# Kernel optimization log

Measured on AMD Instinct MI355X. Metric: run time of the kernel, lower is better.

The kernel has to match this reference:

```python
import jax, jax.numpy as jnp
import numpy as np

B, S, E, H = 4, 2048, 1024, 16
D = E // H


def setup_inputs() -> dict:
    key = jax.random.key(0)
    ks = jax.random.split(key, 8)
    inv = 1.0 / np.sqrt(E)
    return {
        "query": jax.random.normal(ks[0], (B, S, E), dtype=jnp.float32),
        "key": jax.random.normal(ks[1], (B, S, E), dtype=jnp.float32),
        "value": jax.random.normal(ks[2], (B, S, E), dtype=jnp.float32),
        "key_padding_mask": jnp.zeros((B, S), dtype=bool),
        "Wq": jax.random.uniform(ks[3], (E, E), jnp.float32, -inv, inv),
        "Wk": jax.random.uniform(ks[4], (E, E), jnp.float32, -inv, inv),
        "Wv": jax.random.uniform(ks[5], (E, E), jnp.float32, -inv, inv),
        "Wo": jax.random.uniform(ks[6], (E, E), jnp.float32, -inv, inv),
        "gamma": jnp.ones((H,), dtype=jnp.float32),
    }


def reference(query, key, value, key_padding_mask, Wq, Wk, Wv, Wo, gamma):
    b, s, e = query.shape
    h = gamma.shape[0]
    d = e // h
    # torch Linear: x @ W.T ; split into heads -> [b, h, s, d]
    q = (query @ Wq.T).reshape(b, s, h, d).swapaxes(1, 2)
    k = (key @ Wk.T).reshape(b, key.shape[1], h, d).swapaxes(1, 2)
    v = (value @ Wv.T).reshape(b, value.shape[1], h, d).swapaxes(1, 2)
    scores = jnp.einsum("bhqd,bhkd->bhqk", q, k) / jnp.sqrt(jnp.asarray(d, q.dtype))
    scores = jnp.where(key_padding_mask[:, None, None, :], -jnp.inf, scores)
    attn = jax.nn.softmax(scores, axis=-1)  # dropout p=0 in eval-equivalent reference
    out = jnp.einsum("bhqk,bhkd->bhqd", attn, v)
    out = out * gamma[None, :, None, None]  # head-scale
    out = out.swapaxes(1, 2).reshape(b, s, e)
    return out @ Wo.T
```

## Files before the change

kernel.cpp:

```cpp
#include <hip/hip_runtime.h>
#include <hip/hip_bf16.h>
#include <cstdint>

typedef __bf16 bf16;
typedef __bf16 bf16_8 __attribute__((ext_vector_type(8)));
typedef __bf16 bf16_4 __attribute__((ext_vector_type(4)));
typedef float f32_4 __attribute__((ext_vector_type(4)));
typedef short s16x4 __attribute__((ext_vector_type(4)));
typedef short s16x8 __attribute__((ext_vector_type(8)));

#define MFMA_16x16x32(a, b, c) __builtin_amdgcn_mfma_f32_16x16x32_bf16((a), (b), (c), 0, 0, 0)

__device__ __forceinline__ void gll16(const void* g, void* l) {
  __builtin_amdgcn_global_load_lds((const __attribute__((address_space(1))) void*)g,
                                   (__attribute__((address_space(3))) void*)l, 16, 0, 0);
}

__device__ __forceinline__ float exp2fast(float x) {
#if __has_builtin(__builtin_amdgcn_exp2f)
  return __builtin_amdgcn_exp2f(x);
#else
  return __exp2f(x);
#endif
}

__device__ __forceinline__ unsigned bfbits(float x) {
  bf16 b = (bf16)x;
  return (unsigned)__builtin_bit_cast(unsigned short, b);
}

__device__ __forceinline__ bf16_8 cvt8(float4 a, float4 b) {
  bf16_8 v;
  v[0] = (bf16)a.x; v[1] = (bf16)a.y; v[2] = (bf16)a.z; v[3] = (bf16)a.w;
  v[4] = (bf16)b.x; v[5] = (bf16)b.y; v[6] = (bf16)b.z; v[7] = (bf16)b.w;
  return v;
}

__global__ __launch_bounds__(256) void convert4(const float* __restrict__ w0,
                                                const float* __restrict__ w1,
                                                const float* __restrict__ w2,
                                                const float* __restrict__ w3,
                                                bf16* __restrict__ out, int per) {
  const float* srcs[4] = {w0, w1, w2, w3};
  const float* src = srcs[blockIdx.y];
  bf16* dst = out + (size_t)blockIdx.y * per;
  const float sc = (blockIdx.y == 0) ? 0.18033688f : 1.0f;
  int i = (blockIdx.x * 256 + threadIdx.x) * 4;
  float4 f = *(const float4*)(src + i);
  bf16_4 v;
  v[0] = (bf16)(f.x * sc); v[1] = (bf16)(f.y * sc);
  v[2] = (bf16)(f.z * sc); v[3] = (bf16)(f.w * sc);
  *(bf16_4*)(dst + i) = v;
}

__global__ __launch_bounds__(256) void gemm_qkv(const float* __restrict__ Aq,
                                                const float* __restrict__ Ak,
                                                const float* __restrict__ Av,
                                                const bf16* __restrict__ W,
                                                bf16* __restrict__ Qp,
                                                bf16* __restrict__ Kp,
                                                bf16* __restrict__ Vt) {
  constexpr int BM = 128, BK = 32, K = 1024, N = 1024, M_S = 2048;
  __shared__ alignas(16) bf16 As[2][BM * BK];
  __shared__ alignas(16) bf16 Bs[2][BM * BK];

  const int tid = threadIdx.x;
  const int wave = tid >> 6, lane = tid & 63;
  const int quad = lane >> 4, l15 = lane & 15;
  const int wm = (wave & 1) * 64, wn = (wave >> 1) * 64;
  const int tensor = blockIdx.y >> 3;
  const int n0 = (blockIdx.y & 7) * 128;
  const size_t m0 = (size_t)blockIdx.x * BM;

  const float* A = tensor == 0 ? Aq : (tensor == 1 ? Ak : Av);
  const bf16* Bt = W + ((size_t)tensor << 20);

  f32_4 acc[4][4] = {};

  const size_t g_laneoff = (size_t)(lane >> 2) * K + (lane & 3) * 8;
  const float* Ag = A + (m0 + wave * 32) * (size_t)K + g_laneoff;
  const bf16* Bg = Bt + ((size_t)n0 + wave * 32) * (size_t)K + g_laneoff;
  const int l_off = wave * 32 * BK + lane * 8;

  auto stageB = [&](int b, int k0) {
    gll16(Bg + k0, &Bs[b][l_off]);
    gll16(Bg + 16 * (size_t)K + k0, &Bs[b][l_off + 16 * BK]);
  };
  auto loadA = [&](int k0, float4* r) {
    r[0] = *(const float4*)(Ag + k0);
    r[1] = *(const float4*)(Ag + k0 + 4);
    r[2] = *(const float4*)(Ag + 16 * (size_t)K + k0);
    r[3] = *(const float4*)(Ag + 16 * (size_t)K + k0 + 4);
  };
  auto writeA = [&](int b, const float4* r) {
    *(bf16_8*)&As[b][l_off] = cvt8(r[0], r[1]);
    *(bf16_8*)&As[b][l_off + 16 * BK] = cvt8(r[2], r[3]);
  };

  {
    float4 a0[4];
    loadA(0, a0);
    stageB(0, 0);
    writeA(0, a0);
  }
  int buf = 0;
  for (int k0 = 0; k0 < K; k0 += BK, buf ^= 1) {
    __syncthreads();
    const bool more = k0 + BK < K;
    float4 an[4];
    if (more) {
      loadA(k0 + BK, an);
      stageB(buf ^ 1, k0 + BK);
    }

    bf16_8 af[4], bfr[4];
#pragma unroll
    for (int mt = 0; mt < 4; ++mt)
      af[mt] = *(const bf16_8*)&As[buf][(wm + mt * 16 + l15) * BK + quad * 8];
#pragma unroll
    for (int nt = 0; nt < 4; ++nt)
      bfr[nt] = *(const bf16_8*)&Bs[buf][(wn + nt * 16 + l15) * BK + quad * 8];
#pragma unroll
    for (int mt = 0; mt < 4; ++mt)
#pragma unroll
      for (int nt = 0; nt < 4; ++nt)
        acc[mt][nt] = MFMA_16x16x32(af[mt], bfr[nt], acc[mt][nt]);

    if (more) writeA(buf ^ 1, an);
  }

  if (tensor < 2) {
    bf16* C = tensor == 0 ? Qp : Kp;
#pragma unroll
    for (int mt = 0; mt < 4; ++mt)
#pragma unroll
      for (int i = 0; i < 4; ++i) {
        size_t row = m0 + wm + mt * 16 + quad * 4 + i;
        bf16* cr = C + row * N + n0 + wn + l15;
#pragma unroll
        for (int nt = 0; nt < 4; ++nt) cr[nt * 16] = (bf16)acc[mt][nt][i];
      }
  } else {
    const int bb = (int)(m0 >> 11);
    const int sbase = (int)(m0 & 2047) + wm;
#pragma unroll
    for (int mt = 0; mt < 4; ++mt)
#pragma unroll
      for (int nt = 0; nt < 4; ++nt) {
        int col = n0 + wn + nt * 16 + l15;
        bf16_4 pk;
        pk[0] = (bf16)acc[mt][nt][0]; pk[1] = (bf16)acc[mt][nt][1];
        pk[2] = (bf16)acc[mt][nt][2]; pk[3] = (bf16)acc[mt][nt][3];
        bf16* dst = Vt + ((size_t)(bb * 16 + (col >> 6)) * 64 + (col & 63)) * M_S +
                    sbase + (mt >> 1) * 32 + quad * 8 + (mt & 1) * 4;
        *(bf16_4*)dst = pk;
      }
  }
}

__global__ __launch_bounds__(256) void gemm_out(const bf16* __restrict__ A,
                                                const bf16* __restrict__ Bt,
                                                float* __restrict__ C,
                                                int M, int N, int K) {
  constexpr int BM = 128, BN = 128, BK = 32;
  __shared__ alignas(16) bf16 As[2][BM * BK];
  __shared__ alignas(16) bf16 Bs[2][BN * BK];

  const int tid = threadIdx.x;
  const int wave = tid >> 6, lane = tid & 63;
  const int quad = lane >> 4, l15 = lane & 15;
  const int wm = (wave & 1) * 64, wn = (wave >> 1) * 64;
  const size_t m0 = (size_t)blockIdx.x * BM;
  const size_t n0 = (size_t)blockIdx.y * BN;

  f32_4 acc[4][4] = {};

  const size_t g_laneoff = (size_t)(lane >> 2) * K + (lane & 3) * 8;
  const bf16* Ag = A + (m0 + wave * 32) * (size_t)K + g_laneoff;
  const bf16* Bg = Bt + (n0 + wave * 32) * (size_t)K + g_laneoff;
  const int l_off = wave * 32 * BK + lane * 8;

  auto stage = [&](int b, int k0) {
    gll16(Ag + k0, &As[b][l_off]);
    gll16(Ag + 16 * (size_t)K + k0, &As[b][l_off + 16 * BK]);
    gll16(Bg + k0, &Bs[b][l_off]);
    gll16(Bg + 16 * (size_t)K + k0, &Bs[b][l_off + 16 * BK]);
  };

  stage(0, 0);
  int buf = 0;
  for (int k0 = 0; k0 < K; k0 += BK, buf ^= 1) {
    __syncthreads();
    if (k0 + BK < K) stage(buf ^ 1, k0 + BK);

    bf16_8 af[4], bfr[4];
#pragma unroll
    for (int mt = 0; mt < 4; ++mt)
      af[mt] = *(const bf16_8*)&As[buf][(wm + mt * 16 + l15) * BK + quad * 8];
#pragma unroll
    for (int nt = 0; nt < 4; ++nt)
      bfr[nt] = *(const bf16_8*)&Bs[buf][(wn + nt * 16 + l15) * BK + quad * 8];
#pragma unroll
    for (int mt = 0; mt < 4; ++mt)
#pragma unroll
      for (int nt = 0; nt < 4; ++nt)
        acc[mt][nt] = MFMA_16x16x32(af[mt], bfr[nt], acc[mt][nt]);
  }

#pragma unroll
  for (int mt = 0; mt < 4; ++mt)
#pragma unroll
    for (int i = 0; i < 4; ++i) {
      size_t row = m0 + wm + mt * 16 + quad * 4 + i;
      float* cr = C + row * N + n0 + wn + l15;
#pragma unroll
      for (int nt = 0; nt < 4; ++nt) cr[nt * 16] = acc[mt][nt][i];
    }
}

__global__ __launch_bounds__(256, 4) void attn_fused(const bf16* __restrict__ Q,
                                                     const bf16* __restrict__ K,
                                                     const bf16* __restrict__ Vt,
                                                     const unsigned char* __restrict__ mask,
                                                     const float* __restrict__ gamma,
                                                     bf16* __restrict__ Out) {
  constexpr int S = 2048, E = 1024;
  constexpr float NEGB = -3.0e38f;
  __shared__ alignas(16) bf16 Ks[2][64 * 64];
  __shared__ alignas(16) bf16 Vs[2][64 * 64];

  const int tid = threadIdx.x;
  const int wave = tid >> 6, lane = tid & 63;
  const int quad = lane >> 4, l15 = lane & 15;

  const int bx = blockIdx.x, by = blockIdx.y;
  const int wx = (bx >> 3) | ((by & 7) << 1);
  const int bh = (bx & 7) | (by & ~7);
  const int q0 = wx * 128;
  const int b = bh >> 4, h = bh & 15;

  const unsigned char* mg = mask + (size_t)b * S;

  bool anym;
  {
    const uint4* m4 = (const uint4*)mg;
    uint4 x = m4[lane * 2], y = m4[lane * 2 + 1];
    unsigned o = (x.x | x.y | x.z | x.w) | (y.x | y.y | y.z | y.w);
    anym = __ballot(o != 0) != 0ull;
  }

  const int lrow = lane >> 3;
  const int sx = ((lane & 7) ^ lrow) * 8;
  const size_t koff = (size_t)lrow * E + sx;
  const size_t voff = (size_t)lrow * S + sx;

  const bf16* Qg = Q + ((size_t)(b * S + q0)) * E + h * 64;
  const bf16* Kg = K + ((size_t)b * S) * E + h * 64;
  const bf16* Vg = Vt + ((size_t)bh * 64) * S;

  auto stageKV = [&](int bf_, int kt) {
#pragma unroll
    for (int p = 0; p < 2; ++p) {
      gll16(Kg + (size_t)(kt + wave * 16 + p * 8) * E + koff,
            &Ks[bf_][(wave * 16 + p * 8) * 64 + lane * 8]);
      gll16(Vg + (size_t)(wave * 16 + p * 8) * S + voff + kt,
            &Vs[bf_][(wave * 16 + p * 8) * 64 + lane * 8]);
    }
  };

  stageKV(0, 0);

  bf16_8 qf[2][2];
#pragma unroll
  for (int mt = 0; mt < 2; ++mt)
#pragma unroll
    for (int ks = 0; ks < 2; ++ks)
      qf[mt][ks] = *(const bf16_8*)(Qg + (size_t)(wave * 32 + mt * 16 + l15) * E +
                                    ks * 32 + quad * 8);

  s16x8 onesP;
#pragma unroll
  for (int j = 0; j < 8; ++j) onesP[j] = (short)0x3F80;
  const bf16_8 onesA8 = __builtin_bit_cast(bf16_8, onesP);

  f32_4 accO[4][2] = {};
  f32_4 accR[2] = {};

  int buf = 0;
  for (int kt = 0; kt < S; kt += 64, buf ^= 1) {
    __syncthreads();
    if (kt + 64 < S) stageKV(buf ^ 1, kt + 64);

    f32_4 sT[4][2] = {};
#pragma unroll
    for (int ks = 0; ks < 2; ++ks)
#pragma unroll
      for (int t = 0; t < 4; ++t) {
        bf16_8 af = *(const bf16_8*)&Ks[buf][(t * 16 + l15) * 64 +
                                            (((ks * 4 + quad) ^ (l15 & 7)) * 8)];
        sT[t][0] = MFMA_16x16x32(af, qf[0][ks], sT[t][0]);
        sT[t][1] = MFMA_16x16x32(af, qf[1][ks], sT[t][1]);
      }

    s16x4 pk[4][2];
#pragma unroll
    for (int t = 0; t < 4; ++t) {
      float bb0 = 0.0f, bb1 = 0.0f, bb2 = 0.0f, bb3 = 0.0f;
      if (anym) {
        const unsigned um = *(const unsigned*)(mg + kt + t * 16 + quad * 4);
        bb0 = (um & 0xffu) ? NEGB : 0.0f;
        bb1 = (um & 0xff00u) ? NEGB : 0.0f;
        bb2 = (um & 0xff0000u) ? NEGB : 0.0f;
        bb3 = (um & 0xff000000u) ? NEGB : 0.0f;
      }
#pragma unroll
      for (int mt = 0; mt < 2; ++mt) {
        float e0 = exp2fast(sT[t][mt][0] + bb0);
        float e1 = exp2fast(sT[t][mt][1] + bb1);
        float e2 = exp2fast(sT[t][mt][2] + bb2);
        float e3 = exp2fast(sT[t][mt][3] + bb3);
        uint2 u;
        u.x = bfbits(e0) | (bfbits(e1) << 16);
        u.y = bfbits(e2) | (bfbits(e3) << 16);
        pk[t][mt] = __builtin_bit_cast(s16x4, u);
      }
    }

#pragma unroll
    for (int i2 = 0; i2 < 2; ++i2) {
      const bf16_8 pb0 = __builtin_bit_cast(bf16_8,
          __builtin_shufflevector(pk[2 * i2][0], pk[2 * i2 + 1][0], 0, 1, 2, 3, 4, 5, 6, 7));
      const bf16_8 pb1 = __builtin_bit_cast(bf16_8,
          __builtin_shufflevector(pk[2 * i2][1], pk[2 * i2 + 1][1], 0, 1, 2, 3, 4, 5, 6, 7));
      accR[0] = MFMA_16x16x32(onesA8, pb0, accR[0]);
      accR[1] = MFMA_16x16x32(onesA8, pb1, accR[1]);
      const int xo = ((i2 * 4 + quad) ^ (l15 & 7)) * 8;
#pragma unroll
      for (int dt = 0; dt < 4; ++dt) {
        bf16_8 vf = *(const bf16_8*)&Vs[buf][(dt * 16 + l15) * 64 + xo];
        accO[dt][0] = MFMA_16x16x32(vf, pb0, accO[dt][0]);
        accO[dt][1] = MFMA_16x16x32(vf, pb1, accO[dt][1]);
      }
    }
  }

  const float g = gamma[h];
  float invv[2];
#pragma unroll
  for (int mt = 0; mt < 2; ++mt) invv[mt] = g / accR[mt][0];

#pragma unroll
  for (int mt = 0; mt < 2; ++mt) {
    size_t token = (size_t)(b * S) + q0 + wave * 32 + mt * 16 + l15;
    bf16* orow = Out + token * E + h * 64;
#pragma unroll
    for (int dt = 0; dt < 4; ++dt) {
      bf16_4 ov;
      ov[0] = (bf16)(accO[dt][mt][0] * invv[mt]);
      ov[1] = (bf16)(accO[dt][mt][1] * invv[mt]);
      ov[2] = (bf16)(accO[dt][mt][2] * invv[mt]);
      ov[3] = (bf16)(accO[dt][mt][3] * invv[mt]);
      *(bf16_4*)(orow + dt * 16 + quad * 4) = ov;
    }
  }
}

extern "C" void kernel_launch(void* const* d_in, const int* in_sizes, int n_in,
                              void* d_out, int out_size, void* d_ws, size_t ws_size,
                              hipStream_t stream) {
  constexpr int Bb = 4, S = 2048, E = 1024;
  constexpr int M = Bb * S;

  const float* q = (const float*)d_in[0];
  const float* k = (const float*)d_in[1];
  const float* v = (const float*)d_in[2];
  const unsigned char* mask = (const unsigned char*)d_in[3];
  const float* Wq = (const float*)d_in[4];
  const float* Wk = (const float*)d_in[5];
  const float* Wv = (const float*)d_in[6];
  const float* Wo = (const float*)d_in[7];
  const float* gamma = (const float*)d_in[8];

  char* ws = (char*)d_ws;
  bf16* Wb = (bf16*)ws;
  bf16* At = (bf16*)(ws + ((size_t)8 << 20));
  bf16* Vt = (bf16*)(ws + ((size_t)56 << 20));
  bf16* Qp = (bf16*)d_out;
  bf16* Kp = (bf16*)d_out + ((size_t)1 << 23);

  convert4<<<dim3(1024, 4), 256, 0, stream>>>(Wq, Wk, Wv, Wo, Wb, 1 << 20);

  gemm_qkv<<<dim3(M / 128, 24), 256, 0, stream>>>(q, k, v, Wb, Qp, Kp, Vt);

  attn_fused<<<dim3(S / 128, Bb * 16), 256, 0, stream>>>(Qp, Kp, Vt, mask, gamma, At);

  gemm_out<<<dim3(M / 128, E / 128), 256, 0, stream>>>(At, Wb + (3 << 20), (float*)d_out, M, E, E);
}
```

Measured before the change: 396.0 us.

## Pre-convert QKV activations to bf16 and stage both GEMM operands via direct-to-LDS loads

Adds a combined conversion kernel that turns the fp32 query/key/value activations, along with the weights, into bf16 buffers in workspace. The QKV GEMM can then load its A operand with global_load_lds like B, dropping the register round-trip and the in-loop fp32-to-bf16 conversion. The A operand is now read at half the width repeatedly across N tiles, at the cost of one extra full pass over the activations. Separately, the attention kernel raises wave priority around its MFMA blocks with s_setprio.

```diff
diff --git a/kernel.cpp b/kernel.cpp
--- a/kernel.cpp
+++ b/kernel.cpp
@@ -29,33 +29,45 @@
   return (unsigned)__builtin_bit_cast(unsigned short, b);
 }
 
-__device__ __forceinline__ bf16_8 cvt8(float4 a, float4 b) {
-  bf16_8 v;
-  v[0] = (bf16)a.x; v[1] = (bf16)a.y; v[2] = (bf16)a.z; v[3] = (bf16)a.w;
-  v[4] = (bf16)b.x; v[5] = (bf16)b.y; v[6] = (bf16)b.z; v[7] = (bf16)b.w;
-  return v;
-}
-
-__global__ __launch_bounds__(256) void convert4(const float* __restrict__ w0,
-                                                const float* __restrict__ w1,
-                                                const float* __restrict__ w2,
-                                                const float* __restrict__ w3,
-                                                bf16* __restrict__ out, int per) {
-  const float* srcs[4] = {w0, w1, w2, w3};
-  const float* src = srcs[blockIdx.y];
-  bf16* dst = out + (size_t)blockIdx.y * per;
-  const float sc = (blockIdx.y == 0) ? 0.18033688f : 1.0f;
-  int i = (blockIdx.x * 256 + threadIdx.x) * 4;
-  float4 f = *(const float4*)(src + i);
-  bf16_4 v;
-  v[0] = (bf16)(f.x * sc); v[1] = (bf16)(f.y * sc);
-  v[2] = (bf16)(f.z * sc); v[3] = (bf16)(f.w * sc);
-  *(bf16_4*)(dst + i) = v;
-}
-
-__global__ __launch_bounds__(256) void gemm_qkv(const float* __restrict__ Aq,
-                                                const float* __restrict__ Ak,
-                                                const float* __restrict__ Av,
+__global__ __launch_bounds__(256) void cvt_all(const float* __restrict__ q,
+                                               const float* __restrict__ k,
+                                               const float* __restrict__ v,
+                                               const float* __restrict__ w0,
+                                               const float* __restrict__ w1,
+                                               const float* __restrict__ w2,
+                                               const float* __restrict__ w3,
+                                               bf16* __restrict__ qb,
+                                               bf16* __restrict__ kb,
+                                               bf16* __restrict__ vb,
+                                               bf16* __restrict__ wb) {
+  const int y = blockIdx.y;
+  if (y < 3) {
+    const float* src = y == 0 ? q : (y == 1 ? k : v);
+    bf16* dst = y == 0 ? qb : (y == 1 ? kb : vb);
+    size_t i = ((size_t)blockIdx.x * 256 + threadIdx.x) * 8;
+    float4 f0 = *(const float4*)(src + i);
+    float4 f1 = *(const float4*)(src + i + 4);
+    bf16_8 o;
+    o[0] = (bf16)f0.x; o[1] = (bf16)f0.y; o[2] = (bf16)f0.z; o[3] = (bf16)f0.w;
+    o[4] = (bf16)f1.x; o[5] = (bf16)f1.y; o[6] = (bf16)f1.z; o[7] = (bf16)f1.w;
+    *(bf16_8*)(dst + i) = o;
+  } else {
+    size_t i = ((size_t)blockIdx.x * 256 + threadIdx.x) * 4;
+    const int widx = (int)(i >> 20);
+    const size_t off = i & (((size_t)1 << 20) - 1);
+    const float* srcs[4] = {w0, w1, w2, w3};
+    const float sc = (widx == 0) ? 0.18033688f : 1.0f;
+    float4 f = *(const float4*)(srcs[widx] + off);
+    bf16_4 o;
+    o[0] = (bf16)(f.x * sc); o[1] = (bf16)(f.y * sc);
+    o[2] = (bf16)(f.z * sc); o[3] = (bf16)(f.w * sc);
+    *(bf16_4*)(wb + i) = o;
+  }
+}
+
+__global__ __launch_bounds__(256) void gemm_qkv(const bf16* __restrict__ Aq,
+                                                const bf16* __restrict__ Ak,
+                                                const bf16* __restrict__ Av,
                                                 const bf16* __restrict__ W,
                                                 bf16* __restrict__ Qp,
                                                 bf16* __restrict__ Kp,
@@ -72,46 +84,28 @@
   const int n0 = (blockIdx.y & 7) * 128;
   const size_t m0 = (size_t)blockIdx.x * BM;
 
-  const float* A = tensor == 0 ? Aq : (tensor == 1 ? Ak : Av);
+  const bf16* A = tensor == 0 ? Aq : (tensor == 1 ? Ak : Av);
   const bf16* Bt = W + ((size_t)tensor << 20);
 
   f32_4 acc[4][4] = {};
 
   const size_t g_laneoff = (size_t)(lane >> 2) * K + (lane & 3) * 8;
-  const float* Ag = A + (m0 + wave * 32) * (size_t)K + g_laneoff;
+  const bf16* Ag = A + (m0 + wave * 32) * (size_t)K + g_laneoff;
   const bf16* Bg = Bt + ((size_t)n0 + wave * 32) * (size_t)K + g_laneoff;
   const int l_off = wave * 32 * BK + lane * 8;
 
-  auto stageB = [&](int b, int k0) {
+  auto stage = [&](int b, int k0) {
+    gll16(Ag + k0, &As[b][l_off]);
+    gll16(Ag + 16 * (size_t)K + k0, &As[b][l_off + 16 * BK]);
     gll16(Bg + k0, &Bs[b][l_off]);
     gll16(Bg + 16 * (size_t)K + k0, &Bs[b][l_off + 16 * BK]);
   };
-  auto loadA = [&](int k0, float4* r) {
-    r[0] = *(const float4*)(Ag + k0);
-    r[1] = *(const float4*)(Ag + k0 + 4);
-    r[2] = *(const float4*)(Ag + 16 * (size_t)K + k0);
-    r[3] = *(const float4*)(Ag + 16 * (size_t)K + k0 + 4);
-  };
-  auto writeA = [&](int b, const float4* r) {
-    *(bf16_8*)&As[b][l_off] = cvt8(r[0], r[1]);
-    *(bf16_8*)&As[b][l_off + 16 * BK] = cvt8(r[2], r[3]);
-  };
-
-  {
-    float4 a0[4];
-    loadA(0, a0);
-    stageB(0, 0);
-    writeA(0, a0);
-  }
+
+  stage(0, 0);
   int buf = 0;
   for (int k0 = 0; k0 < K; k0 += BK, buf ^= 1) {
     __syncthreads();
-    const bool more = k0 + BK < K;
-    float4 an[4];
-    if (more) {
-      loadA(k0 + BK, an);
-      stageB(buf ^ 1, k0 + BK);
-    }
+    if (k0 + BK < K) stage(buf ^ 1, k0 + BK);
 
     bf16_8 af[4], bfr[4];
 #pragma unroll
@@ -125,8 +119,6 @@
 #pragma unroll
       for (int nt = 0; nt < 4; ++nt)
         acc[mt][nt] = MFMA_16x16x32(af[mt], bfr[nt], acc[mt][nt]);
-
-    if (more) writeA(buf ^ 1, an);
   }
 
   if (tensor < 2) {
@@ -292,6 +284,7 @@
     if (kt + 64 < S) stageKV(buf ^ 1, kt + 64);
 
     f32_4 sT[4][2] = {};
+    __builtin_amdgcn_s_setprio(1);
 #pragma unroll
     for (int ks = 0; ks < 2; ++ks)
 #pragma unroll
@@ -301,6 +294,7 @@
         sT[t][0] = MFMA_16x16x32(af, qf[0][ks], sT[t][0]);
         sT[t][1] = MFMA_16x16x32(af, qf[1][ks], sT[t][1]);
       }
+    __builtin_amdgcn_s_setprio(0);
 
     s16x4 pk[4][2];
 #pragma unroll
@@ -326,6 +320,7 @@
       }
     }
 
+    __builtin_amdgcn_s_setprio(1);
 #pragma unroll
     for (int i2 = 0; i2 < 2; ++i2) {
       const bf16_8 pb0 = __builtin_bit_cast(bf16_8,
@@ -342,6 +337,7 @@
         accO[dt][1] = MFMA_16x16x32(vf, pb1, accO[dt][1]);
       }
     }
+    __builtin_amdgcn_s_setprio(0);
   }
 
   const float g = gamma[h];
@@ -383,15 +379,18 @@
 
   char* ws = (char*)d_ws;
   bf16* Wb = (bf16*)ws;
-  bf16* At = (bf16*)(ws + ((size_t)8 << 20));
+  bf16* qb = (bf16*)(ws + ((size_t)8 << 20));
+  bf16* kb = (bf16*)(ws + ((size_t)24 << 20));
+  bf16* vb = (bf16*)(ws + ((size_t)40 << 20));
   bf16* Vt = (bf16*)(ws + ((size_t)56 << 20));
   bf16* Qp = (bf16*)d_out;
   bf16* Kp = (bf16*)d_out + ((size_t)1 << 23);
 
-  convert4<<<dim3(1024, 4), 256, 0, stream>>>(Wq, Wk, Wv, Wo, Wb, 1 << 20);
-
-  gemm_qkv<<<dim3(M / 128, 24), 256, 0, stream>>>(q, k, v, Wb, Qp, Kp, Vt);
-
+  cvt_all<<<dim3(4096, 4), 256, 0, stream>>>(q, k, v, Wq, Wk, Wv, Wo, qb, kb, vb, Wb);
+
+  gemm_qkv<<<dim3(M / 128, 24), 256, 0, stream>>>(qb, kb, vb, Wb, Qp, Kp, Vt);
+
+  bf16* At = qb;
   attn_fused<<<dim3(S / 128, Bb * 16), 256, 0, stream>>>(Qp, Kp, Vt, mask, gamma, At);
 
   gemm_out<<<dim3(M / 128, E / 128), 256, 0, stream>>>(At, Wb + (3 << 20), (float*)d_out, M, E, E);
```

Result: faster. 337.8 us (-14.7%).
